# Performance work log

Measured on AMD Instinct MI355X. Metric: run time of the kernel, lower is better.

Reference implementation:

```python
import jax, jax.numpy as jnp
import numpy as np

N_NODES = 100000
BASE_DIM = 128
E1 = 500000
E2 = 250000
N_TYPES = 4


def setup_inputs() -> dict:
    key = jax.random.key(0)
    ks = jax.random.split(key, 9)
    x = jax.random.normal(ks[0], (N_NODES, BASE_DIM), dtype=jnp.float32)
    # per-edge-type dense transforms (shape-1: d->d, shape-2: 2d->d)
    W1 = jax.random.normal(ks[1], (N_TYPES, BASE_DIM, BASE_DIM), dtype=jnp.float32) * 0.05
    W2 = jax.random.normal(ks[2], (N_TYPES, 2 * BASE_DIM, BASE_DIM), dtype=jnp.float32) * 0.05
    src1 = jax.random.randint(ks[3], (E1,), 0, N_NODES, dtype=jnp.int32)
    tgt1 = jax.random.randint(ks[4], (E1,), 0, N_NODES, dtype=jnp.int32)
    type1 = jax.random.randint(ks[5], (E1,), 0, N_TYPES, dtype=jnp.int32)
    src2 = jax.random.randint(ks[6], (2 * E2,), 0, N_NODES, dtype=jnp.int32)
    tgt2 = jax.random.randint(ks[7], (E2,), 0, N_NODES, dtype=jnp.int32)
    type2 = jax.random.randint(ks[8], (E2,), 0, N_TYPES, dtype=jnp.int32)
    return {"x": x, "W1": W1, "W2": W2, "src1": src1, "tgt1": tgt1,
            "type1": type1, "src2": src2, "tgt2": tgt2, "type2": type2}


def _gather_transform_scatter(x, W, src, tgt, etype, arity, n_nodes):
    # gather `arity` source nodes per hyperedge and concat features: (E, arity*d)
    d = x.shape[1]
    concat = x[src].reshape(-1, arity * d)
    # per-edge-type dense transform; small loop over fixed #types, masked accumulate
    acc = jnp.zeros((concat.shape[0], d), dtype=x.dtype)
    for t in range(W.shape[0]):
        acc = acc + jnp.where((etype == t)[:, None], concat @ W[t], 0.0)
    # scatter-add messages to target nodes
    return jax.ops.segment_sum(acc, tgt, num_segments=n_nodes)


def reference(x, W1, W2, src1, tgt1, type1, src2, tgt2, type2):
    n = x.shape[0]
    out = x
    out = out + _gather_transform_scatter(x, W1, src1, tgt1, type1, 1, n)
    out = out + _gather_transform_scatter(x, W2, src2, tgt2, type2, 2, n)
    return out
```

## Files before the change

### kernel.cpp

```cpp
#include <hip/hip_runtime.h>
#include <hip/hip_bf16.h>

#define D 128
#define EPB 32
#define NB 256
#define RMASK ((1 << 27) - 1)

typedef __attribute__((ext_vector_type(8))) short bf16x8;
typedef __attribute__((ext_vector_type(4))) float f32x4;

__device__ inline unsigned short f2bf(float f) {
    union { float f; unsigned int u; } v;
    v.f = f;
    unsigned int u = v.u;
    unsigned int r = u + 0x7fffu + ((u >> 16) & 1u);
    return (unsigned short)(r >> 16);
}
__device__ inline float bf2f(unsigned short b) {
    union { unsigned int u; float f; } v;
    v.u = ((unsigned int)b) << 16;
    return v.f;
}
__device__ inline float bflo(unsigned u) { return bf2f((unsigned short)(u & 0xffff)); }
__device__ inline float bfhi(unsigned u) { return bf2f((unsigned short)(u >> 16)); }

__global__ __launch_bounds__(256) void copy_kernel(float* __restrict__ out,
                                                   const float* __restrict__ x,
                                                   int n_elems) {
    int n4 = n_elems >> 2;
    const float4* src = (const float4*)x;
    float4* dst = (float4*)out;
    for (int i = blockIdx.x * blockDim.x + threadIdx.x; i < n4;
         i += gridDim.x * blockDim.x)
        dst[i] = src[i];
}

__global__ __launch_bounds__(256) void conv_w(const float* __restrict__ W,
                                              unsigned short* __restrict__ Wt,
                                              int K) {
    __shared__ float tile[32][33];
    int k0 = blockIdx.x * 32, c0 = blockIdx.y * 32, t = blockIdx.z;
    int tr = threadIdx.x >> 5, tc = threadIdx.x & 31;
#pragma unroll
    for (int m = 0; m < 4; m++)
        tile[m * 8 + tr][tc] = W[((size_t)t * K + k0 + m * 8 + tr) * D + c0 + tc];
    __syncthreads();
#pragma unroll
    for (int m = 0; m < 4; m++)
        Wt[((size_t)t * D + c0 + m * 8 + tr) * K + k0 + tc] = f2bf(tile[tc][m * 8 + tr]);
}

__global__ __launch_bounds__(256) void hist_types(const int* __restrict__ type,
                                                  int n, int* __restrict__ hist) {
    __shared__ int h[4];
    if (threadIdx.x < 4) h[threadIdx.x] = 0;
    __syncthreads();
    for (int i = blockIdx.x * 256 + threadIdx.x; i < n; i += NB * 256)
        atomicAdd(&h[type[i]], 1);
    __syncthreads();
    if (threadIdx.x < 4) hist[blockIdx.x * 4 + threadIdx.x] = h[threadIdx.x];
}

__global__ void scan_offsets(int* __restrict__ meta,
                             const int* __restrict__ hist1, int* __restrict__ off1,
                             const int* __restrict__ hist2, int* __restrict__ off2) {
    int t = threadIdx.x;
    if (t < 4) {
        int s = 0;
        for (int b = 0; b < NB; b++) s += hist1[b * 4 + t];
        meta[t] = s;
    } else if (t < 8) {
        int tt = t - 4, s = 0;
        for (int b = 0; b < NB; b++) s += hist2[b * 4 + tt];
        meta[4 + tt] = s;
    }
    __syncthreads();
    if (t == 0) {
        int p = 0;
        for (int k = 0; k < 4; k++) {
            meta[8 + k] = p;
            p += ((meta[k] + EPB - 1) / EPB) * EPB;
        }
        meta[12] = p;
        p = 0;
        for (int k = 0; k < 4; k++) {
            meta[13 + k] = p;
            p += ((meta[4 + k] + EPB - 1) / EPB) * EPB;
        }
        meta[17] = p;
    }
    __syncthreads();
    if (t < 4) {
        int p = meta[8 + t];
        for (int b = 0; b < NB; b++) { off1[b * 4 + t] = p; p += hist1[b * 4 + t]; }
    } else if (t < 8) {
        int tt = t - 4;
        int p = meta[13 + tt];
        for (int b = 0; b < NB; b++) { off2[b * 4 + tt] = p; p += hist2[b * 4 + tt]; }
    }
}

__global__ __launch_bounds__(256) void write_sorted(const int* __restrict__ type,
                                                    int n,
                                                    const int* __restrict__ off,
                                                    int* __restrict__ sorted) {
    __shared__ int loff[4];
    if (threadIdx.x < 4) loff[threadIdx.x] = off[blockIdx.x * 4 + threadIdx.x];
    __syncthreads();
    for (int i = blockIdx.x * 256 + threadIdx.x; i < n; i += NB * 256) {
        int t = type[i];
        int pos = atomicAdd(&loff[t], 1);
        sorted[pos] = i;
    }
}

__global__ __launch_bounds__(256) void assign_rel(const int* __restrict__ tgt, int n,
                                                  int* __restrict__ cnt,
                                                  int* __restrict__ pos) {
    for (int i = blockIdx.x * blockDim.x + threadIdx.x; i < n;
         i += gridDim.x * blockDim.x)
        pos[i] = atomicAdd(&cnt[tgt[i]], 1);
}

__global__ __launch_bounds__(256) void scan_pass1(const int* __restrict__ cnt, int n,
                                                  int* __restrict__ base,
                                                  int* __restrict__ bsum) {
    __shared__ int s[256];
    int b = blockIdx.x, t = threadIdx.x;
    int i0 = b * 512 + 2 * t;
    int v0 = (i0 < n) ? cnt[i0] : 0;
    int v1 = (i0 + 1 < n) ? cnt[i0 + 1] : 0;
    s[t] = v0 + v1;
    __syncthreads();
    for (int off = 1; off < 256; off <<= 1) {
        int v = s[t];
        int u = (t >= off) ? s[t - off] : 0;
        __syncthreads();
        s[t] = v + u;
        __syncthreads();
    }
    int excl = (t > 0) ? s[t - 1] : 0;
    if (i0 < n) base[i0] = excl;
    if (i0 + 1 < n) base[i0 + 1] = excl + v0;
    if (t == 255) bsum[b] = s[255];
}

__global__ __launch_bounds__(256) void scan_pass2(int* __restrict__ bsum, int nb) {
    __shared__ int s[256];
    int t = threadIdx.x;
    int run = 0;
    for (int b0 = 0; b0 < nb; b0 += 256) {
        int v = (b0 + t < nb) ? bsum[b0 + t] : 0;
        s[t] = v;
        __syncthreads();
        for (int off = 1; off < 256; off <<= 1) {
            int a = s[t];
            int u = (t >= off) ? s[t - off] : 0;
            __syncthreads();
            s[t] = a + u;
            __syncthreads();
        }
        if (b0 + t < nb) bsum[b0 + t] = run + ((t > 0) ? s[t - 1] : 0);
        int tot = s[255];
        __syncthreads();
        run += tot;
    }
    if (t == 0) bsum[nb] = run;
}

__global__ __launch_bounds__(256) void scan_pass3(int* __restrict__ base,
                                                  const int* __restrict__ bsum, int n) {
    int i = blockIdx.x * 256 + threadIdx.x;
    if (i < n) base[i] += bsum[i >> 9];
    else if (i == n) base[n] = bsum[(n + 511) >> 9];
}

__global__ __launch_bounds__(256) void write_rec1(
    const int* __restrict__ src, const int* __restrict__ tgt,
    const int* __restrict__ type, int n, const int* __restrict__ base,
    const int* __restrict__ pos, int* __restrict__ rec) {
    for (int i = blockIdx.x * blockDim.x + threadIdx.x; i < n;
         i += gridDim.x * blockDim.x)
        rec[base[tgt[i]] + pos[i]] = src[i] | (type[i] << 27);
}

__global__ __launch_bounds__(256) void write_rec2(
    const int* __restrict__ src2, const int* __restrict__ tgt,
    const int* __restrict__ type, int n, const int* __restrict__ base,
    const int* __restrict__ pos, int* __restrict__ reca, int* __restrict__ recb) {
    for (int i = blockIdx.x * blockDim.x + threadIdx.x; i < n;
         i += gridDim.x * blockDim.x) {
        int s = base[tgt[i]] + pos[i];
        reca[s] = src2[2 * i] | (type[i] << 27);
        recb[s] = src2[2 * i + 1];
    }
}

__global__ __launch_bounds__(256) void dense_tab(
    const float* __restrict__ x, const unsigned short* __restrict__ wt,
    unsigned short* __restrict__ tabs, int nn, int stage) {
    __shared__ unsigned short Cs[128 * 128];
    char* Csb = (char*)Cs;
    int tid = threadIdx.x;
    int wave = tid >> 6, lane = tid & 63;
    int lrow = lane & 15, lgrp = lane >> 4;
    int m0 = blockIdx.x * 128;
    int r0 = wave * 32;

    bf16x8 a[2][4];
#pragma unroll
    for (int fr = 0; fr < 2; fr++) {
        int rr = m0 + r0 + fr * 16 + lrow;
        bool ok = rr < nn;
        const float* xr = x + (size_t)rr * D;
#pragma unroll
        for (int kk = 0; kk < 4; kk++) {
            float4 p0 = make_float4(0.f, 0.f, 0.f, 0.f), p1 = p0;
            if (ok) {
                p0 = *(const float4*)(xr + kk * 32 + lgrp * 8);
                p1 = *(const float4*)(xr + kk * 32 + lgrp * 8 + 4);
            }
            union { bf16x8 v; unsigned short s[8]; } u;
            u.s[0] = f2bf(p0.x); u.s[1] = f2bf(p0.y);
            u.s[2] = f2bf(p0.z); u.s[3] = f2bf(p0.w);
            u.s[4] = f2bf(p1.x); u.s[5] = f2bf(p1.y);
            u.s[6] = f2bf(p1.z); u.s[7] = f2bf(p1.w);
            a[fr][kk] = u.v;
        }
    }

    int ng = stage ? 8 : 4;
    int K = stage ? 2 * D : D;
    for (int g = 0; g < ng; g++) {
        int t = g & 3;
        int koff = stage ? ((g >> 2) * D) : 0;
        const unsigned short* W = wt + (size_t)t * D * K;
        unsigned short* tab = tabs + (size_t)g * nn * D;

        for (int cf = 0; cf < 4; cf++) {
            int c0 = cf * 32;
            bf16x8 b[2][4];
#pragma unroll
            for (int fc = 0; fc < 2; fc++)
#pragma unroll
                for (int kk = 0; kk < 4; kk++)
                    b[fc][kk] = *(const bf16x8*)(W + (size_t)(c0 + fc * 16 + lrow) * K +
                                                 koff + kk * 32 + lgrp * 8);
            f32x4 acc[2][2];
#pragma unroll
            for (int i = 0; i < 2; i++)
#pragma unroll
                for (int j = 0; j < 2; j++) acc[i][j] = (f32x4){0.f, 0.f, 0.f, 0.f};
#pragma unroll
            for (int kk = 0; kk < 4; kk++) {
                acc[0][0] = __builtin_amdgcn_mfma_f32_16x16x32_bf16(a[0][kk], b[0][kk], acc[0][0], 0, 0, 0);
                acc[1][0] = __builtin_amdgcn_mfma_f32_16x16x32_bf16(a[1][kk], b[0][kk], acc[1][0], 0, 0, 0);
                acc[0][1] = __builtin_amdgcn_mfma_f32_16x16x32_bf16(a[0][kk], b[1][kk], acc[0][1], 0, 0, 0);
                acc[1][1] = __builtin_amdgcn_mfma_f32_16x16x32_bf16(a[1][kk], b[1][kk], acc[1][1], 0, 0, 0);
            }
#pragma unroll
            for (int fr = 0; fr < 2; fr++)
#pragma unroll
                for (int reg = 0; reg < 4; reg++) {
                    int row = r0 + fr * 16 + lgrp * 4 + reg;
#pragma unroll
                    for (int fc = 0; fc < 2; fc++) {
                        int col = c0 + fc * 16 + lrow;
                        *(unsigned short*)(Csb + row * 256 +
                                           ((col * 2) ^ ((row & 7) << 4))) =
                            f2bf(acc[fr][fc][reg]);
                    }
                }
        }
#pragma unroll
        for (int it = 0; it < 8; it++) {
            int flat = lane + it * 64;
            int row = r0 + (flat >> 4), j = flat & 15;
            if (m0 + row < nn)
                *(uint4*)(tab + ((size_t)(m0 + row)) * D + j * 8) =
                    *(const uint4*)(Csb + row * 256 + ((j ^ (row & 7)) * 16));
        }
    }
}

__global__ __launch_bounds__(256) void gather1(
    const float* __restrict__ x, const unsigned short* __restrict__ tabs,
    const int* __restrict__ base1, const int* __restrict__ rec1,
    float* __restrict__ out, int nn) {
    int wib = threadIdx.x >> 6, lane = threadIdx.x & 63;
    for (int v = blockIdx.x * 4 + wib; v < nn; v += gridDim.x * 4) {
        float2 xv = *(const float2*)(x + (size_t)v * D + lane * 2);
        float a0 = xv.x, a1 = xv.y;
        int b0 = base1[v], b1 = base1[v + 1];
        int i = b0;
        for (; i + 1 < b1; i += 2) {
            int r0 = rec1[i], r1 = rec1[i + 1];
            const unsigned short* p0 =
                tabs + ((size_t)((unsigned)r0 >> 27) * nn + (r0 & RMASK)) * D;
            const unsigned short* p1 =
                tabs + ((size_t)((unsigned)r1 >> 27) * nn + (r1 & RMASK)) * D;
            unsigned u0 = *(const unsigned*)(p0 + lane * 2);
            unsigned u1 = *(const unsigned*)(p1 + lane * 2);
            a0 += bflo(u0) + bflo(u1);
            a1 += bfhi(u0) + bfhi(u1);
        }
        if (i < b1) {
            int r0 = rec1[i];
            const unsigned short* p0 =
                tabs + ((size_t)((unsigned)r0 >> 27) * nn + (r0 & RMASK)) * D;
            unsigned u0 = *(const unsigned*)(p0 + lane * 2);
            a0 += bflo(u0);
            a1 += bfhi(u0);
        }
        *(float2*)(out + (size_t)v * D + lane * 2) = make_float2(a0, a1);
    }
}

__global__ __launch_bounds__(256) void gather2(
    const unsigned short* __restrict__ tabs,
    const int* __restrict__ base2, const int* __restrict__ rec2a,
    const int* __restrict__ rec2b, float* __restrict__ out, int nn) {
    int wib = threadIdx.x >> 6, lane = threadIdx.x & 63;
    for (int v = blockIdx.x * 4 + wib; v < nn; v += gridDim.x * 4) {
        int c0 = base2[v], c1 = base2[v + 1];
        if (c0 == c1) continue;
        float2 ov = *(const float2*)(out + (size_t)v * D + lane * 2);
        float a0 = ov.x, a1 = ov.y;
        for (int j = c0; j < c1; j++) {
            int ra = rec2a[j], sb = rec2b[j];
            int t = (int)((unsigned)ra >> 27), sa = ra & RMASK;
            const unsigned short* pu = tabs + ((size_t)t * nn + sa) * D;
            const unsigned short* pl = tabs + ((size_t)(4 + t) * nn + sb) * D;
            unsigned uu = *(const unsigned*)(pu + lane * 2);
            unsigned ul = *(const unsigned*)(pl + lane * 2);
            a0 += bflo(uu) + bflo(ul);
            a1 += bfhi(uu) + bfhi(ul);
        }
        *(float2*)(out + (size_t)v * D + lane * 2) = make_float2(a0, a1);
    }
}

__global__ __launch_bounds__(256) void edge1_msg(
    const float* __restrict__ x, const unsigned short* __restrict__ Wt1,
    const int* __restrict__ src, const int* __restrict__ tgt,
    const int* __restrict__ sorted, const int* __restrict__ meta,
    const int* __restrict__ basep, const int* __restrict__ pos,
    unsigned short* __restrict__ msg) {
    __shared__ uint4 As4[512];
    __shared__ int s_mrow[EPB];
    __shared__ int s_src[EPB];
    char* As = (char*)As4;

    int tid = threadIdx.x;
    int g0 = blockIdx.x * EPB;
    const int* pb = meta + 8;
    int t = 0;
#pragma unroll
    for (int k = 1; k < 4; k++)
        if (g0 >= pb[k]) t = k;
    const unsigned short* __restrict__ W = Wt1 + (size_t)t * D * D;

    if (tid < EPB) {
        int eid = sorted[g0 + tid];
        int sv = -1, mr = -1;
        if (eid >= 0) { sv = src[eid]; mr = basep[tgt[eid]] + pos[eid]; }
        s_src[tid] = sv;
        s_mrow[tid] = mr;
    }
    __syncthreads();
    {
        int r = tid >> 3, u0 = tid & 7;
        int sv = s_src[r];
        const float4* srow = (const float4*)(x + (size_t)sv * D);
#pragma unroll
        for (int q = 0; q < 4; q++) {
            int u = u0 + 8 * q;
            float4 v = make_float4(0.f, 0.f, 0.f, 0.f);
            if (sv >= 0) v = srow[u];
            uint2 p;
            p.x = (unsigned)f2bf(v.x) | ((unsigned)f2bf(v.y) << 16);
            p.y = (unsigned)f2bf(v.z) | ((unsigned)f2bf(v.w) << 16);
            int byte = ((((u >> 1) * 16) ^ ((r & 7) << 4)) + (u & 1) * 8);
            *(uint2*)(As + r * 256 + byte) = p;
        }
    }
    __syncthreads();

    int wave = tid >> 6, lane = tid & 63;
    int c0 = wave * 32;
    int lrow = lane & 15, lgrp = lane >> 4;

    bf16x8 b[2][4];
#pragma unroll
    for (int fc = 0; fc < 2; fc++)
#pragma unroll
        for (int kk = 0; kk < 4; kk++)
            b[fc][kk] = *(const bf16x8*)(W + (size_t)(c0 + fc * 16 + lrow) * D +
                                         kk * 32 + lgrp * 8);

    f32x4 acc[2][2];
#pragma unroll
    for (int i = 0; i < 2; i++)
#pragma unroll
        for (int j = 0; j < 2; j++) acc[i][j] = (f32x4){0.f, 0.f, 0.f, 0.f};

#pragma unroll
    for (int kk = 0; kk < 4; kk++) {
        bf16x8 a0, a1;
        {
            int r = lrow;
            a0 = *(const bf16x8*)(As + r * 256 + ((kk * 64 + lgrp * 16) ^ ((r & 7) << 4)));
        }
        {
            int r = 16 + lrow;
            a1 = *(const bf16x8*)(As + r * 256 + ((kk * 64 + lgrp * 16) ^ ((r & 7) << 4)));
        }
        acc[0][0] = __builtin_amdgcn_mfma_f32_16x16x32_bf16(a0, b[0][kk], acc[0][0], 0, 0, 0);
        acc[1][0] = __builtin_amdgcn_mfma_f32_16x16x32_bf16(a1, b[0][kk], acc[1][0], 0, 0, 0);
        acc[0][1] = __builtin_amdgcn_mfma_f32_16x16x32_bf16(a0, b[1][kk], acc[0][1], 0, 0, 0);
        acc[1][1] = __builtin_amdgcn_mfma_f32_16x16x32_bf16(a1, b[1][kk], acc[1][1], 0, 0, 0);
    }

#pragma unroll
    for (int fr = 0; fr < 2; fr++)
#pragma unroll
        for (int reg = 0; reg < 4; reg++) {
            int erow = fr * 16 + lgrp * 4 + reg;
            int mr = s_mrow[erow];
            if (mr >= 0) {
#pragma unroll
                for (int fc = 0; fc < 2; fc++)
                    msg[(size_t)mr * D + c0 + fc * 16 + lrow] = f2bf(acc[fr][fc][reg]);
            }
        }
}

__global__ __launch_bounds__(256) void edge2_msg(
    const float* __restrict__ x, const unsigned short* __restrict__ Wt2,
    const int* __restrict__ src2, const int* __restrict__ tgt,
    const int* __restrict__ sorted, const int* __restrict__ meta,
    const int* __restrict__ basep, const int* __restrict__ pos,
    unsigned short* __restrict__ msg) {
    __shared__ uint4 As4[1024];
    __shared__ int s_mrow[EPB];
    __shared__ int s_srcA[EPB];
    __shared__ int s_srcB[EPB];
    char* As = (char*)As4;

    int tid = threadIdx.x;
    int g0 = blockIdx.x * EPB;
    const int* pb = meta + 13;
    int t = 0;
#pragma unroll
    for (int k = 1; k < 4; k++)
        if (g0 >= pb[k]) t = k;
    const unsigned short* __restrict__ W = Wt2 + (size_t)t * D * 2 * D;

    if (tid < EPB) {
        int eid = sorted[g0 + tid];
        int sa = -1, sb = -1, mr = -1;
        if (eid >= 0) {
            sa = src2[2 * eid];
            sb = src2[2 * eid + 1];
            mr = basep[tgt[eid]] + pos[eid];
        }
        s_srcA[tid] = sa;
        s_srcB[tid] = sb;
        s_mrow[tid] = mr;
    }
    __syncthreads();
    {
        int r = tid >> 3, u0 = tid & 7;
        int sa = s_srcA[r], sb = s_srcB[r];
        const float4* rowA = (const float4*)(x + (size_t)sa * D);
        const float4* rowB = (const float4*)(x + (size_t)sb * D);
#pragma unroll
        for (int q = 0; q < 8; q++) {
            int u = u0 + 8 * q;
            float4 v = make_float4(0.f, 0.f, 0.f, 0.f);
            if (sa >= 0) v = (u < 32) ? rowA[u] : rowB[u - 32];
            uint2 p;
            p.x = (unsigned)f2bf(v.x) | ((unsigned)f2bf(v.y) << 16);
            p.y = (unsigned)f2bf(v.z) | ((unsigned)f2bf(v.w) << 16);
            int byte = ((((u >> 1) * 16) ^ ((r & 7) << 4)) + (u & 1) * 8);
            *(uint2*)(As + r * 512 + byte) = p;
        }
    }
    __syncthreads();

    int wave = tid >> 6, lane = tid & 63;
    int c0 = wave * 32;
    int lrow = lane & 15, lgrp = lane >> 4;

    f32x4 acc[2][2];
#pragma unroll
    for (int i = 0; i < 2; i++)
#pragma unroll
        for (int j = 0; j < 2; j++) acc[i][j] = (f32x4){0.f, 0.f, 0.f, 0.f};

#pragma unroll
    for (int kk = 0; kk < 8; kk++) {
        bf16x8 b0 = *(const bf16x8*)(W + (size_t)(c0 + lrow) * 2 * D + kk * 32 + lgrp * 8);
        bf16x8 b1 = *(const bf16x8*)(W + (size_t)(c0 + 16 + lrow) * 2 * D + kk * 32 + lgrp * 8);
        bf16x8 a0, a1;
        {
            int r = lrow;
            a0 = *(const bf16x8*)(As + r * 512 + ((kk * 64 + lgrp * 16) ^ ((r & 7) << 4)));
        }
        {
            int r = 16 + lrow;
            a1 = *(const bf16x8*)(As + r * 512 + ((kk * 64 + lgrp * 16) ^ ((r & 7) << 4)));
        }
        acc[0][0] = __builtin_amdgcn_mfma_f32_16x16x32_bf16(a0, b0, acc[0][0], 0, 0, 0);
        acc[1][0] = __builtin_amdgcn_mfma_f32_16x16x32_bf16(a1, b0, acc[1][0], 0, 0, 0);
        acc[0][1] = __builtin_amdgcn_mfma_f32_16x16x32_bf16(a0, b1, acc[0][1], 0, 0, 0);
        acc[1][1] = __builtin_amdgcn_mfma_f32_16x16x32_bf16(a1, b1, acc[1][1], 0, 0, 0);
    }

#pragma unroll
    for (int fr = 0; fr < 2; fr++)
#pragma unroll
        for (int reg = 0; reg < 4; reg++) {
            int erow = fr * 16 + lgrp * 4 + reg;
            int mr = s_mrow[erow];
            if (mr >= 0) {
#pragma unroll
                for (int fc = 0; fc < 2; fc++)
                    msg[(size_t)mr * D + c0 + fc * 16 + lrow] = f2bf(acc[fr][fc][reg]);
            }
        }
}

__global__ __launch_bounds__(256) void finalize(
    const float* __restrict__ x, const unsigned short* __restrict__ msg,
    const int* __restrict__ basep, float* __restrict__ out, int nn) {
    int wib = threadIdx.x >> 6, lane = threadIdx.x & 63;
    for (int v = blockIdx.x * 4 + wib; v < nn; v += gridDim.x * 4) {
        int b0 = basep[v], b1 = basep[v + 1];
        float2 xv = *(const float2*)(x + (size_t)v * D + lane * 2);
        float a0 = xv.x, a1 = xv.y;
        for (int i = b0; i < b1; i++) {
            unsigned u = *(const unsigned*)(msg + (size_t)i * D + lane * 2);
            a0 += bflo(u);
            a1 += bfhi(u);
        }
        *(float2*)(out + (size_t)v * D + lane * 2) = make_float2(a0, a1);
    }
}

__global__ __launch_bounds__(256) void e1_simple(
    const float* __restrict__ x, const float* __restrict__ W1,
    const int* __restrict__ src, const int* __restrict__ tgt,
    const int* __restrict__ type, float* __restrict__ out, int n) {
    int lane = threadIdx.x & 63;
    int wid = (blockIdx.x * blockDim.x + threadIdx.x) >> 6;
    int nw = (gridDim.x * blockDim.x) >> 6;
    for (int e = wid; e < n; e += nw) {
        const float* W = W1 + (size_t)type[e] * D * D;
        const float* xr = x + (size_t)src[e] * D;
        float a0 = 0.f, a1 = 0.f;
        for (int i = 0; i < D; i++) {
            float xv = xr[i];
            a0 = fmaf(xv, W[i * D + lane], a0);
            a1 = fmaf(xv, W[i * D + 64 + lane], a1);
        }
        atomicAdd(&out[(size_t)tgt[e] * D + lane], a0);
        atomicAdd(&out[(size_t)tgt[e] * D + 64 + lane], a1);
    }
}

__global__ __launch_bounds__(256) void e2_simple(
    const float* __restrict__ x, const float* __restrict__ W2,
    const int* __restrict__ src2, const int* __restrict__ tgt,
    const int* __restrict__ type, float* __restrict__ out, int n) {
    int lane = threadIdx.x & 63;
    int wid = (blockIdx.x * blockDim.x + threadIdx.x) >> 6;
    int nw = (gridDim.x * blockDim.x) >> 6;
    for (int e = wid; e < n; e += nw) {
        const float* W = W2 + (size_t)type[e] * 2 * D * D;
        const float* xrA = x + (size_t)src2[2 * e] * D;
        const float* xrB = x + (size_t)src2[2 * e + 1] * D;
        float a0 = 0.f, a1 = 0.f;
        for (int i = 0; i < 2 * D; i++) {
            float xv = (i < D) ? xrA[i] : xrB[i - D];
            a0 = fmaf(xv, W[i * D + lane], a0);
            a1 = fmaf(xv, W[i * D + 64 + lane], a1);
        }
        atomicAdd(&out[(size_t)tgt[e] * D + lane], a0);
        atomicAdd(&out[(size_t)tgt[e] * D + 64 + lane], a1);
    }
}

extern "C" void kernel_launch(void* const* d_in, const int* in_sizes, int n_in,
                              void* d_out, int out_size, void* d_ws, size_t ws_size,
                              hipStream_t stream) {
    const float* x = (const float*)d_in[0];
    const float* W1 = (const float*)d_in[1];
    const float* W2 = (const float*)d_in[2];
    const int* src1 = (const int*)d_in[3];
    const int* tgt1 = (const int*)d_in[4];
    const int* type1 = (const int*)d_in[5];
    const int* src2 = (const int*)d_in[6];
    const int* tgt2 = (const int*)d_in[7];
    const int* type2 = (const int*)d_in[8];
    float* out = (float*)d_out;

    int nn = in_sizes[0] / D;
    int E1c = in_sizes[3];
    int E2c = in_sizes[7];

    int nb_scan = (nn + 511) / 512;
    size_t w1_elems = (size_t)4 * D * D;
    size_t w2_elems = (size_t)4 * D * 2 * D;
    size_t wt_bytes = (w1_elems + w2_elems) * 2;

    size_t o_cnt1 = 0;
    size_t o_cnt2 = o_cnt1 + nn;
    size_t o_base1 = o_cnt2 + nn;
    size_t o_base2 = o_base1 + nn + 1;
    size_t o_bsum1 = o_base2 + nn + 1;
    size_t o_bsum2 = o_bsum1 + nb_scan + 1;
    size_t o_pos1d = o_bsum2 + nb_scan + 1;
    size_t o_pos2d = o_pos1d + E1c;
    size_t o_rec1 = o_pos2d + E2c;
    size_t o_rec2a = o_rec1 + E1c;
    size_t o_rec2b = o_rec2a + E2c;
    size_t ints_dense = o_rec2b + E2c;
    size_t wtd_off = (ints_dense * 4 + 255) & ~(size_t)255;
    size_t tab_off = (wtd_off + wt_bytes + 255) & ~(size_t)255;
    size_t tab_bytes = (size_t)8 * nn * D * 2;
    size_t need_dense = tab_off + tab_bytes;

    int grid1 = (E1c + 4 * (EPB - 1) + EPB - 1) / EPB;
    int grid2 = (E2c + 4 * (EPB - 1) + EPB - 1) / EPB;
    int cap1 = grid1 * EPB;
    int cap2 = grid2 * EPB;
    size_t o_meta = 0;
    size_t o_hist1 = o_meta + 32;
    size_t o_off1 = o_hist1 + (size_t)NB * 4;
    size_t o_hist2 = o_off1 + (size_t)NB * 4;
    size_t o_off2 = o_hist2 + (size_t)NB * 4;
    size_t o_sorted1 = o_off2 + (size_t)NB * 4;
    size_t o_sorted2 = o_sorted1 + cap1;
    size_t o_pos1 = o_sorted2 + cap2;
    size_t o_pos2 = o_pos1 + E1c;
    size_t o_cnt = o_pos2 + E2c;
    size_t o_base = o_cnt + nn;
    size_t o_bsum = o_base + nn + 1;
    size_t ints_full = o_bsum + nb_scan + 1;
    size_t wb_full = (ints_full * 4 + 255) & ~(size_t)255;
    size_t msg_off = (wb_full + wt_bytes + 255) & ~(size_t)255;
    size_t msg_bytes = (size_t)(E1c + E2c) * D * 2;
    size_t need_full = msg_off + msg_bytes;

    if (ws_size >= need_dense && nn < (1 << 27)) {
        int* wsI = (int*)d_ws;
        int* cnt1 = wsI + o_cnt1;
        int* cnt2 = wsI + o_cnt2;
        int* base1 = wsI + o_base1;
        int* base2 = wsI + o_base2;
        int* bsum1 = wsI + o_bsum1;
        int* bsum2 = wsI + o_bsum2;
        int* pos1 = wsI + o_pos1d;
        int* pos2 = wsI + o_pos2d;
        int* rec1 = wsI + o_rec1;
        int* rec2a = wsI + o_rec2a;
        int* rec2b = wsI + o_rec2b;
        unsigned short* wt1 = (unsigned short*)((char*)d_ws + wtd_off);
        unsigned short* wt2 = wt1 + w1_elems;
        unsigned short* tabs = (unsigned short*)((char*)d_ws + tab_off);

        hipMemsetAsync(cnt1, 0, (size_t)8 * nn, stream);

        conv_w<<<dim3(4, 4, 4), 256, 0, stream>>>(W1, wt1, D);
        conv_w<<<dim3(8, 4, 4), 256, 0, stream>>>(W2, wt2, 2 * D);

        assign_rel<<<2048, 256, 0, stream>>>(tgt1, E1c, cnt1, pos1);
        assign_rel<<<2048, 256, 0, stream>>>(tgt2, E2c, cnt2, pos2);

        scan_pass1<<<nb_scan, 256, 0, stream>>>(cnt1, nn, base1, bsum1);
        scan_pass2<<<1, 256, 0, stream>>>(bsum1, nb_scan);
        scan_pass3<<<(nn + 1 + 255) / 256, 256, 0, stream>>>(base1, bsum1, nn);
        scan_pass1<<<nb_scan, 256, 0, stream>>>(cnt2, nn, base2, bsum2);
        scan_pass2<<<1, 256, 0, stream>>>(bsum2, nb_scan);
        scan_pass3<<<(nn + 1 + 255) / 256, 256, 0, stream>>>(base2, bsum2, nn);

        write_rec1<<<2048, 256, 0, stream>>>(src1, tgt1, type1, E1c, base1, pos1, rec1);
        write_rec2<<<2048, 256, 0, stream>>>(src2, tgt2, type2, E2c, base2, pos2,
                                             rec2a, rec2b);

        int gblk = (nn + 127) / 128;
        dense_tab<<<gblk, 256, 0, stream>>>(x, wt1, tabs, nn, 0);
        gather1<<<(nn + 3) / 4, 256, 0, stream>>>(x, tabs, base1, rec1, out, nn);
        dense_tab<<<gblk, 256, 0, stream>>>(x, wt2, tabs, nn, 1);
        gather2<<<(nn + 3) / 4, 256, 0, stream>>>(tabs, base2, rec2a, rec2b, out, nn);
    } else if (ws_size >= need_full) {
        int* wsI = (int*)d_ws;
        int* meta = wsI + o_meta;
        int* hist1 = wsI + o_hist1;
        int* off1 = wsI + o_off1;
        int* hist2 = wsI + o_hist2;
        int* off2 = wsI + o_off2;
        int* sorted1 = wsI + o_sorted1;
        int* sorted2 = wsI + o_sorted2;
        int* pos1 = wsI + o_pos1;
        int* pos2 = wsI + o_pos2;
        int* cnt = wsI + o_cnt;
        int* basep = wsI + o_base;
        int* bsum = wsI + o_bsum;
        unsigned short* wt1 = (unsigned short*)((char*)d_ws + wb_full);
        unsigned short* wt2 = wt1 + w1_elems;
        unsigned short* msg = (unsigned short*)((char*)d_ws + msg_off);

        hipMemsetAsync(sorted1, 0xFF, (size_t)4 * (cap1 + cap2), stream);
        hipMemsetAsync(cnt, 0, (size_t)4 * nn, stream);

        conv_w<<<dim3(4, 4, 4), 256, 0, stream>>>(W1, wt1, D);
        conv_w<<<dim3(8, 4, 4), 256, 0, stream>>>(W2, wt2, 2 * D);

        hist_types<<<NB, 256, 0, stream>>>(type1, E1c, hist1);
        hist_types<<<NB, 256, 0, stream>>>(type2, E2c, hist2);
        scan_offsets<<<1, 64, 0, stream>>>(meta, hist1, off1, hist2, off2);
        write_sorted<<<NB, 256, 0, stream>>>(type1, E1c, off1, sorted1);
        write_sorted<<<NB, 256, 0, stream>>>(type2, E2c, off2, sorted2);

        assign_rel<<<2048, 256, 0, stream>>>(tgt1, E1c, cnt, pos1);
        assign_rel<<<2048, 256, 0, stream>>>(tgt2, E2c, cnt, pos2);
        scan_pass1<<<nb_scan, 256, 0, stream>>>(cnt, nn, basep, bsum);
        scan_pass2<<<1, 256, 0, stream>>>(bsum, nb_scan);
        scan_pass3<<<(nn + 1 + 255) / 256, 256, 0, stream>>>(basep, bsum, nn);

        edge1_msg<<<grid1, 256, 0, stream>>>(x, wt1, src1, tgt1, sorted1, meta,
                                             basep, pos1, msg);
        edge2_msg<<<grid2, 256, 0, stream>>>(x, wt2, src2, tgt2, sorted2, meta,
                                             basep, pos2, msg);
        finalize<<<(nn + 3) / 4, 256, 0, stream>>>(x, msg, basep, out, nn);
    } else {
        copy_kernel<<<2048, 256, 0, stream>>>(out, x, nn * D);
        e1_simple<<<2048, 256, 0, stream>>>(x, W1, src1, tgt1, type1, out, E1c);
        e2_simple<<<2048, 256, 0, stream>>>(x, W2, src2, tgt2, type2, out, E2c);
    }
}
```

Baseline: 391.3 us.

## Store dense tables in permuted column layout directly from MFMA registers

```diff
diff --git a/kernel.cpp b/kernel.cpp
--- a/kernel.cpp
+++ b/kernel.cpp
@@ -199,8 +199,6 @@
 __global__ __launch_bounds__(256) void dense_tab(
     const float* __restrict__ x, const unsigned short* __restrict__ wt,
     unsigned short* __restrict__ tabs, int nn, int stage) {
-    __shared__ unsigned short Cs[128 * 128];
-    char* Csb = (char*)Cs;
     int tid = threadIdx.x;
     int wave = tid >> 6, lane = tid & 63;
     int lrow = lane & 15, lgrp = lane >> 4;
@@ -237,6 +235,7 @@
         const unsigned short* W = wt + (size_t)t * D * K;
         unsigned short* tab = tabs + (size_t)g * nn * D;
 
+#pragma unroll
         for (int cf = 0; cf < 4; cf++) {
             int c0 = cf * 32;
             bf16x8 b[2][4];
@@ -262,23 +261,13 @@
             for (int fr = 0; fr < 2; fr++)
 #pragma unroll
                 for (int reg = 0; reg < 4; reg++) {
-                    int row = r0 + fr * 16 + lgrp * 4 + reg;
-#pragma unroll
-                    for (int fc = 0; fc < 2; fc++) {
-                        int col = c0 + fc * 16 + lrow;
-                        *(unsigned short*)(Csb + row * 256 +
-                                           ((col * 2) ^ ((row & 7) << 4))) =
-                            f2bf(acc[fr][fc][reg]);
+                    int row = m0 + r0 + fr * 16 + lgrp * 4 + reg;
+                    if (row < nn) {
+                        unsigned pv = (unsigned)f2bf(acc[fr][0][reg]) |
+                                      ((unsigned)f2bf(acc[fr][1][reg]) << 16);
+                        *(unsigned*)(tab + (size_t)row * D + lrow * 8 + cf * 2) = pv;
                     }
                 }
-        }
-#pragma unroll
-        for (int it = 0; it < 8; it++) {
-            int flat = lane + it * 64;
-            int row = r0 + (flat >> 4), j = flat & 15;
-            if (m0 + row < nn)
-                *(uint4*)(tab + ((size_t)(m0 + row)) * D + j * 8) =
-                    *(const uint4*)(Csb + row * 256 + ((j ^ (row & 7)) * 16));
         }
     }
 }
@@ -288,9 +277,11 @@
     const int* __restrict__ base1, const int* __restrict__ rec1,
     float* __restrict__ out, int nn) {
     int wib = threadIdx.x >> 6, lane = threadIdx.x & 63;
+    int cl = (lane & 3) * 32 + (lane >> 2);
+    int ch = cl + 16;
     for (int v = blockIdx.x * 4 + wib; v < nn; v += gridDim.x * 4) {
-        float2 xv = *(const float2*)(x + (size_t)v * D + lane * 2);
-        float a0 = xv.x, a1 = xv.y;
+        float a0 = x[(size_t)v * D + cl];
+        float a1 = x[(size_t)v * D + ch];
         int b0 = base1[v], b1 = base1[v + 1];
         int i = b0;
         for (; i + 1 < b1; i += 2) {
@@ -312,7 +303,8 @@
             a0 += bflo(u0);
             a1 += bfhi(u0);
         }
-        *(float2*)(out + (size_t)v * D + lane * 2) = make_float2(a0, a1);
+        out[(size_t)v * D + cl] = a0;
+        out[(size_t)v * D + ch] = a1;
     }
 }
 
@@ -321,11 +313,13 @@
     const int* __restrict__ base2, const int* __restrict__ rec2a,
     const int* __restrict__ rec2b, float* __restrict__ out, int nn) {
     int wib = threadIdx.x >> 6, lane = threadIdx.x & 63;
+    int cl = (lane & 3) * 32 + (lane >> 2);
+    int ch = cl + 16;
     for (int v = blockIdx.x * 4 + wib; v < nn; v += gridDim.x * 4) {
         int c0 = base2[v], c1 = base2[v + 1];
         if (c0 == c1) continue;
-        float2 ov = *(const float2*)(out + (size_t)v * D + lane * 2);
-        float a0 = ov.x, a1 = ov.y;
+        float a0 = out[(size_t)v * D + cl];
+        float a1 = out[(size_t)v * D + ch];
         for (int j = c0; j < c1; j++) {
             int ra = rec2a[j], sb = rec2b[j];
             int t = (int)((unsigned)ra >> 27), sa = ra & RMASK;
@@ -336,7 +330,8 @@
             a0 += bflo(uu) + bflo(ul);
             a1 += bfhi(uu) + bfhi(ul);
         }
-        *(float2*)(out + (size_t)v * D + lane * 2) = make_float2(a0, a1);
+        out[(size_t)v * D + cl] = a0;
+        out[(size_t)v * D + ch] = a1;
     }
 }
 
```

Result: slower. 493.3 us (+26.1%).
